# Optimization experiments

Hardware: AMD Instinct MI355X
Metric: run time of the kernel (lower is better)

## Reference

```python
import jax, jax.numpy as jnp
import numpy as np
from jax import lax

OUT = 24
THRESHOLD = 0.7
IOU_THRESHOLD = 0.5


def _conv(x, w, b):
    # x: [N,C,H,W], w: [O,I,kh,kw] (torch OIHW), valid padding, stride 1
    y = lax.conv_general_dilated(x, w, (1, 1), 'VALID',
                                 dimension_numbers=('NCHW', 'OIHW', 'NCHW'))
    return y + b[None, :, None, None]


def _prelu(x, a):
    a = a.reshape((1, -1) + (1,) * (x.ndim - 2))
    return jnp.where(x > 0, x, a * x)


def _maxpool(x, k, s, p):
    return lax.reduce_window(x, -jnp.inf, lax.max,
                             (1, 1, k, k), (1, 1, s, s),
                             [(0, 0), (0, 0), (p, p), (p, p)])


def _crop_resize(img, bboxes):
    # img: [3,H,W]; nearest-neighbor resize of each (clipped) crop to 24x24,
    # matching F.interpolate default nearest mode: src = floor(dst*in/out).
    _, H, W = img.shape
    x1 = jnp.clip(bboxes[:, 0].astype(jnp.int32), 0, W)
    y1 = jnp.clip(bboxes[:, 1].astype(jnp.int32), 0, H)
    x2 = jnp.clip(bboxes[:, 2].astype(jnp.int32), 0, W)
    y2 = jnp.clip(bboxes[:, 3].astype(jnp.int32), 0, H)
    j = jnp.arange(OUT)
    ix = jnp.clip(x1[:, None] + (j[None, :] * (x2 - x1)[:, None]) // OUT, 0, W - 1)  # [N,24]
    iy = jnp.clip(y1[:, None] + (j[None, :] * (y2 - y1)[:, None]) // OUT, 0, H - 1)  # [N,24]
    crops = img[:, iy[:, :, None], ix[:, None, :]]  # [3,N,24,24]
    return jnp.transpose(crops, (1, 0, 2, 3))        # [N,3,24,24]


def _pairwise_iou(b):
    x1 = jnp.maximum(b[:, None, 0], b[None, :, 0])
    y1 = jnp.maximum(b[:, None, 1], b[None, :, 1])
    x2 = jnp.minimum(b[:, None, 2], b[None, :, 2])
    y2 = jnp.minimum(b[:, None, 3], b[None, :, 3])
    inter = jnp.clip(x2 - x1, 0) * jnp.clip(y2 - y1, 0)
    area = jnp.clip(b[:, 2] - b[:, 0], 0) * jnp.clip(b[:, 3] - b[:, 1], 0)
    return inter / jnp.maximum(area[:, None] + area[None, :] - inter, 1e-12)


def _nms_keep(boxes, scores, valid, iou_thr):
    # Fixed-shape greedy NMS: returns boolean keep mask over original order.
    N = boxes.shape[0]
    order = jnp.argsort(-scores)
    b = boxes[order]
    v = valid[order]
    iou = _pairwise_iou(b)
    idx = jnp.arange(N)

    def body(i, supp):
        alive = v[i] & jnp.logical_not(supp[i])
        kill = alive & (iou[i] > iou_thr) & (idx > i)
        return supp | kill

    supp = lax.fori_loop(0, N, body, jnp.zeros((N,), bool))
    keep_sorted = v & jnp.logical_not(supp)
    return jnp.zeros((N,), bool).at[order].set(keep_sorted)


def _forward(image, bboxes, conv1_w, conv1_b, prelu1_a, conv2_w, conv2_b, prelu2_a,
             conv3_w, conv3_b, prelu3_a, lin4_w, lin4_b, prelu4_a,
             lin5a_w, lin5a_b, lin5b_w, lin5b_b):
    img = jnp.transpose((image - 127.5) * 0.0078125, (2, 0, 1))  # preprocess, HWC->CHW
    x = _crop_resize(img, bboxes)                                 # [N,3,24,24]
    x = _maxpool(_prelu(_conv(x, conv1_w, conv1_b), prelu1_a), 3, 2, 1)   # [N,28,11,11]
    x = _maxpool(_prelu(_conv(x, conv2_w, conv2_b), prelu2_a), 3, 2, 0)   # [N,48,4,4]
    x = _prelu(_conv(x, conv3_w, conv3_b), prelu3_a)                      # [N,64,3,3]
    x = x.reshape(x.shape[0], -1)                                          # [N,576]
    x = _prelu(x @ lin4_w.T + lin4_b, prelu4_a)                            # [N,128]
    cls = jax.nn.softmax(x @ lin5a_w.T + lin5a_b, axis=1)
    reg = x @ lin5b_w.T + lin5b_b
    scores = cls[:, 1]
    w = bboxes[:, 2] - bboxes[:, 0]
    h = bboxes[:, 3] - bboxes[:, 1]
    boxes = jnp.stack([bboxes[:, 0] + reg[:, 0] * w,
                       bboxes[:, 1] + reg[:, 1] * h,
                       bboxes[:, 2] + reg[:, 2] * w,
                       bboxes[:, 3] + reg[:, 3] * h], axis=1)
    return boxes, scores


def setup_inputs() -> dict:
    key = jax.random.key(0)
    ks = jax.random.split(key, 20)
    H, W, N = 1080, 1920, 4096
    image = jax.random.uniform(ks[0], (H, W, 3), jnp.float32, 0.0, 255.0)
    x1 = jax.random.randint(ks[1], (N,), 0, W - 96).astype(jnp.float32)
    y1 = jax.random.randint(ks[2], (N,), 0, H - 96).astype(jnp.float32)
    bw = jax.random.randint(ks[3], (N,), 24, 96).astype(jnp.float32)
    bh = jax.random.randint(ks[4], (N,), 24, 96).astype(jnp.float32)
    bboxes = jnp.stack([x1, y1, x1 + bw, y1 + bh], axis=1)

    def w(k, shape, scale):
        return jax.random.normal(k, shape, jnp.float32) * scale

    return dict(
        image=image, bboxes=bboxes,
        conv1_w=w(ks[5], (28, 3, 3, 3), 0.1), conv1_b=w(ks[6], (28,), 0.01),
        prelu1_a=jnp.full((28,), 0.25, jnp.float32),
        conv2_w=w(ks[7], (48, 28, 3, 3), 0.06), conv2_b=w(ks[8], (48,), 0.01),
        prelu2_a=jnp.full((48,), 0.25, jnp.float32),
        conv3_w=w(ks[9], (64, 48, 2, 2), 0.07), conv3_b=w(ks[10], (64,), 0.01),
        prelu3_a=jnp.full((64,), 0.25, jnp.float32),
        lin4_w=w(ks[11], (128, 576), 0.04), lin4_b=w(ks[12], (128,), 0.01),
        prelu4_a=jnp.full((128,), 0.25, jnp.float32),
        lin5a_w=w(ks[13], (2, 128), 0.2), lin5a_b=w(ks[14], (2,), 0.01),
        lin5b_w=w(ks[15], (4, 128), 0.09), lin5b_b=w(ks[16], (4,), 0.01),
    )


def reference(image, bboxes, conv1_w, conv1_b, prelu1_a, conv2_w, conv2_b, prelu2_a,
              conv3_w, conv3_b, prelu3_a, lin4_w, lin4_b, prelu4_a,
              lin5a_w, lin5a_b, lin5b_w, lin5b_b):
    boxes, scores = _forward(image, bboxes, conv1_w, conv1_b, prelu1_a,
                             conv2_w, conv2_b, prelu2_a, conv3_w, conv3_b, prelu3_a,
                             lin4_w, lin4_b, prelu4_a, lin5a_w, lin5a_b, lin5b_w, lin5b_b)
    valid = scores >= THRESHOLD
    keep = _nms_keep(boxes, scores, valid, IOU_THRESHOLD)
    # padded (masked) form of `bboxes[pick, :]` so output shape is static
    return jnp.where(keep[:, None], boxes, 0.0)
```

## Files before the change

### kernel.cpp

```cpp
#include <hip/hip_runtime.h>

typedef unsigned long long ull;
typedef __attribute__((ext_vector_type(8))) short bf16x8;
typedef __attribute__((ext_vector_type(4))) float f32x4;

#define W_IMG 1920
#define H_IMG 1080
#define NBOX 4096

#define S_CROP  0
#define S_WT1   2016
#define S_POOL1 5736
#define S_BUF2  3696
#define S_POOL2 7584
#define S_FEAT  0
#define S_VEC   576
#define S_LOUT  704
#define SMEM_F  9432

#define WS_BT   2277392

__device__ __forceinline__ float4 ld4(const float* p) { return *(const float4*)p; }
__device__ __forceinline__ float prelu_f(float v, float a) { return v > 0.f ? v : a * v; }
__device__ __forceinline__ unsigned short bf16rn(float v) {
  unsigned u = __float_as_uint(v);
  return (unsigned short)((u + 0x7fffu + ((u >> 16) & 1u)) >> 16);
}
__device__ __forceinline__ float bf16tof(unsigned short h) {
  return __uint_as_float(((unsigned)h) << 16);
}

__global__ __launch_bounds__(256) void wconv_kernel(const float* __restrict__ w2,
                                                    unsigned short* __restrict__ bt) {
  int tid = threadIdx.x;
  for (int e = tid; e < 13824; e += 256) {
    int c = e & 31, rest = e >> 5;
    int co = rest % 48, kk = rest / 48;
    float v = (c < 28) ? w2[co*252 + c*9 + kk] : 0.f;
    unsigned short h1 = bf16rn(v);
    unsigned short h2 = bf16rn(v - bf16tof(h1));
    bt[e] = h1;
    bt[13824 + e] = h2;
  }
}

template<int SHIFT, int PMIN>
__device__ __forceinline__ void conv1_pool_task(const float* sm, int cq, int y0, int a0,
                                                float* mx) {
#pragma unroll
  for (int wy = 0; wy < 3; ++wy) {
    int y = y0 + wy;
    if (y < 0) continue;
    float acc0[3] = {0.f,0.f,0.f}, acc1[3] = {0.f,0.f,0.f};
    float acc2[3] = {0.f,0.f,0.f}, acc3[3] = {0.f,0.f,0.f};
#pragma unroll
    for (int c = 0; c < 3; ++c) {
#pragma unroll
      for (int kyy = 0; kyy < 3; ++kyy) {
        float r[8];
        const float* src = sm + S_CROP + c*672 + (y + kyy)*28 + a0;
        *(float4*)&r[0] = ld4(src);
        *(float4*)&r[4] = ld4(src + 4);
#pragma unroll
        for (int kxx = 0; kxx < 3; ++kxx) {
          float4 wq = ld4(sm + S_WT1 + (c*9 + kyy*3 + kxx)*32 + cq*4);
#pragma unroll
          for (int wx = PMIN; wx < 3; ++wx) {
            float v = r[SHIFT + wx + kxx];
            acc0[wx] += v*wq.x; acc1[wx] += v*wq.y;
            acc2[wx] += v*wq.z; acc3[wx] += v*wq.w;
          }
        }
      }
    }
#pragma unroll
    for (int wx = PMIN; wx < 3; ++wx) {
      mx[0] = fmaxf(mx[0], acc0[wx]);
      mx[1] = fmaxf(mx[1], acc1[wx]);
      mx[2] = fmaxf(mx[2], acc2[wx]);
      mx[3] = fmaxf(mx[3], acc3[wx]);
    }
  }
}

__global__ __launch_bounds__(256, 4) void cnn_kernel(
    const float* __restrict__ image, const float* __restrict__ bboxes,
    const float* __restrict__ w1, const float* __restrict__ b1, const float* __restrict__ a1,
    const unsigned short* __restrict__ wbt,
    const float* __restrict__ b2, const float* __restrict__ a2,
    const float* __restrict__ w3, const float* __restrict__ b3, const float* __restrict__ a3,
    const float* __restrict__ w4, const float* __restrict__ b4, const float* __restrict__ a4,
    const float* __restrict__ w5a, const float* __restrict__ b5a,
    const float* __restrict__ w5b, const float* __restrict__ b5b,
    float* __restrict__ boxes, float* __restrict__ scores)
{
  __shared__ float sm[SMEM_F];
  __shared__ int s_ix[24], s_iy[24];
  const int tid = threadIdx.x;
  const int n = blockIdx.x;
  const float lo = -__builtin_inff();

  if (tid < 24) {
    int x1 = min(max((int)bboxes[n*4+0], 0), W_IMG);
    int x2 = min(max((int)bboxes[n*4+2], 0), W_IMG);
    s_ix[tid] = min(max(x1 + (tid*(x2-x1))/24, 0), W_IMG-1);
  } else if (tid >= 64 && tid < 88) {
    int j = tid - 64;
    int y1 = min(max((int)bboxes[n*4+1], 0), H_IMG);
    int y2 = min(max((int)bboxes[n*4+3], 0), H_IMG);
    s_iy[j] = min(max(y1 + (j*(y2-y1))/24, 0), H_IMG-1);
  }
  for (int d = tid; d < 756; d += 256) {
    int k = d / 28, co = d % 28;
    sm[S_WT1 + k*32 + co] = w1[co*27 + k];
  }
  __syncthreads();
  for (int e = tid; e < 1728; e += 256) {
    int c = e / 576, rr = e % 576, y = rr / 24, x = rr % 24;
    float v = image[(s_iy[y]*W_IMG + s_ix[x])*3 + c];
    sm[S_CROP + c*672 + y*28 + x] = (v - 127.5f) * 0.0078125f;
  }
  __syncthreads();

  {
    const int wv = tid >> 6, lane = tid & 63;
#pragma unroll 1
    for (int k = 0; k < 4; ++k) {
      const int s = 4*k + wv;
      float mx[4] = {lo, lo, lo, lo};
      int cq, py, px;
      bool valid;
      if (s < 7) {
        int idx = s*64 + lane;
        valid = idx < 385;
        cq = idx % 7; int q = idx / 7; if (q > 54) q = 54;
        py = q / 5; px = 2*(q % 5) + 1;
        conv1_pool_task<1,0>(sm, cq, 2*py - 1, (2*px - 1) & ~3, mx);
      } else if (s < 14) {
        int idx = (s - 7)*64 + lane;
        valid = idx < 385;
        cq = idx % 7; int q = idx / 7; if (q > 54) q = 54;
        py = q / 5; px = 2*(q % 5) + 2;
        conv1_pool_task<3,0>(sm, cq, 2*py - 1, (2*px - 1) & ~3, mx);
      } else {
        int idx = (s - 14)*64 + lane;
        valid = idx < 77;
        cq = idx % 7; py = idx / 7; if (py > 10) py = 10;
        px = 0;
        conv1_pool_task<-1,1>(sm, cq, 2*py - 1, 0, mx);
      }
      if (valid) {
        float4 bq = ld4(&b1[cq*4]);
        float4 aq = ld4(&a1[cq*4]);
        sm[S_POOL1 + (cq*4+0)*132 + py*12 + px] = prelu_f(mx[0] + bq.x, aq.x);
        sm[S_POOL1 + (cq*4+1)*132 + py*12 + px] = prelu_f(mx[1] + bq.y, aq.y);
        sm[S_POOL1 + (cq*4+2)*132 + py*12 + px] = prelu_f(mx[2] + bq.z, aq.z);
        sm[S_POOL1 + (cq*4+3)*132 + py*12 + px] = prelu_f(mx[3] + bq.w, aq.w);
      }
    }
  }
  __syncthreads();

  {
    unsigned short* pl = (unsigned short*)sm;
    for (int e = tid; e < 3696; e += 256) {
      float v = sm[S_POOL1 + e];
      int c = e / 132, rem = e - c*132;
      int it = rem*28 + c;
      unsigned short h1 = bf16rn(v);
      pl[it] = h1;
      pl[3696 + it] = bf16rn(v - bf16tof(h1));
    }
  }
  __syncthreads();

  {
    const int wv = tid >> 6, lane = tid & 63;
    const int grp = lane >> 4, lr = lane & 15;
    const unsigned short* pl = (const unsigned short*)sm;
    const bf16x8* bt = (const bf16x8*)wbt;
#pragma unroll 1
    for (int t = wv; t < 18; t += 4) {
      const int mtile = t / 3, ntile = t - 3*(t/3);
      const int co = ntile*16 + lr;
      const int arow = min(mtile*16 + lr, 80);
      const int oy = (arow*57) >> 9;
      const int ox = arow - 9*oy;
      const int pixb = (oy*12 + ox)*28 + grp*8;
      f32x4 acc = {0.f, 0.f, 0.f, 0.f};
#pragma unroll
      for (int kk = 0; kk < 9; ++kk) {
        const int ky = kk / 3, kx = kk - 3*(kk/3);
        const int aoff = pixb + (ky*12 + kx)*28;
        union { bf16x8 v; ull d[2]; } A1, A2;
        A1.d[0] = *(const ull*)(pl + aoff);
        A1.d[1] = *(const ull*)(pl + aoff + 4);
        A2.d[0] = *(const ull*)(pl + 3696 + aoff);
        A2.d[1] = *(const ull*)(pl + 3696 + aoff + 4);
        const bf16x8 B1 = bt[(kk*48 + co)*4 + grp];
        const bf16x8 B2 = bt[1728 + (kk*48 + co)*4 + grp];
        acc = __builtin_amdgcn_mfma_f32_16x16x32_bf16(A1.v, B2, acc, 0, 0, 0);
        acc = __builtin_amdgcn_mfma_f32_16x16x32_bf16(A2.v, B1, acc, 0, 0, 0);
        acc = __builtin_amdgcn_mfma_f32_16x16x32_bf16(A1.v, B1, acc, 0, 0, 0);
      }
      const float bb = b2[co], aa = a2[co];
      const int p0 = mtile*16 + grp*4;
#pragma unroll
      for (int r = 0; r < 4; ++r) {
        int p = p0 + r;
        if (p < 81) sm[S_BUF2 + co*81 + p] = prelu_f(acc[r] + bb, aa);
      }
    }
  }
  __syncthreads();

  for (int o = tid; o < 768; o += 256) {
    int cl = o >> 4, rem = o & 15, pyy = rem >> 2, pxx = rem & 3;
    float m = lo;
#pragma unroll
    for (int ky = 0; ky < 3; ++ky)
#pragma unroll
      for (int kx = 0; kx < 3; ++kx)
        m = fmaxf(m, sm[S_BUF2 + cl*81 + (2*pyy+ky)*9 + (2*pxx+kx)]);
    sm[S_POOL2 + o] = m;
  }
  __syncthreads();

  {
    int co = tid >> 2, c4 = tid & 3;
    float acc[9] = {};
    for (int cc = 0; cc < 12; ++cc) {
      int c = c4*12 + cc;
      float r[16];
      *(float4*)&r[0]  = ld4(sm + S_POOL2 + c*16);
      *(float4*)&r[4]  = ld4(sm + S_POOL2 + c*16 + 4);
      *(float4*)&r[8]  = ld4(sm + S_POOL2 + c*16 + 8);
      *(float4*)&r[12] = ld4(sm + S_POOL2 + c*16 + 12);
      float4 wq = ld4(&w3[co*192 + c*4]);
#pragma unroll
      for (int p = 0; p < 9; ++p) {
        int pyy = p / 3, pxx = p % 3;
        acc[p] += r[pyy*4+pxx]*wq.x + r[pyy*4+pxx+1]*wq.y
                + r[(pyy+1)*4+pxx]*wq.z + r[(pyy+1)*4+pxx+1]*wq.w;
      }
    }
#pragma unroll
    for (int p = 0; p < 9; ++p) {
      acc[p] += __shfl_xor(acc[p], 1, 64);
      acc[p] += __shfl_xor(acc[p], 2, 64);
    }
    if (c4 == 0) {
      float bb = b3[co], aa = a3[co];
#pragma unroll
      for (int p = 0; p < 9; ++p) sm[S_FEAT + co*9 + p] = prelu_f(acc[p] + bb, aa);
    }
  }
  __syncthreads();

  {
    int wv = tid >> 6, lane = tid & 63;
    for (int f = wv; f < 128; f += 4) {
      const float* wr = w4 + f*576;
      float acc = 0.f;
#pragma unroll
      for (int i = 0; i < 9; ++i) {
        int j = i*64 + lane;
        acc += wr[j] * sm[S_FEAT + j];
      }
#pragma unroll
      for (int off = 1; off < 64; off <<= 1) acc += __shfl_xor(acc, off, 64);
      if (lane == 0) sm[S_VEC + f] = prelu_f(acc + b4[f], a4[f]);
    }
  }
  __syncthreads();

  if (tid < 6) {
    const float* wr = (tid < 2) ? (w5a + tid*128) : (w5b + (tid-2)*128);
    float acc = 0.f;
#pragma unroll
    for (int j = 0; j < 32; ++j) {
      float4 xv = ld4(sm + S_VEC + j*4);
      float4 wv = ld4(wr + j*4);
      acc += xv.x*wv.x + xv.y*wv.y + xv.z*wv.z + xv.w*wv.w;
    }
    acc += (tid < 2) ? b5a[tid] : b5b[tid-2];
    sm[S_LOUT + tid] = acc;
  }
  __syncthreads();
  if (tid == 0) {
    float l0 = sm[S_LOUT+0], l1 = sm[S_LOUT+1];
    float m = fmaxf(l0, l1);
    float e0 = expf(l0 - m), e1 = expf(l1 - m);
    float sc = e1 / (e0 + e1);
    float4 bb = ld4(&bboxes[n*4]);
    float bw = bb.z - bb.x, bh = bb.w - bb.y;
    float4 ob = make_float4(bb.x + sm[S_LOUT+2]*bw, bb.y + sm[S_LOUT+3]*bh,
                            bb.z + sm[S_LOUT+4]*bw, bb.w + sm[S_LOUT+5]*bh);
    *(float4*)&boxes[n*4] = ob;
    scores[n] = sc;
  }
}

__global__ __launch_bounds__(1024) void sort_kernel(const float* __restrict__ scores,
                                                    const float* __restrict__ boxes,
                                                    int* __restrict__ order,
                                                    float* __restrict__ sboxes,
                                                    int* __restrict__ Vp) {
  __shared__ ull keys[NBOX];
  __shared__ int cnt;
  int tid = threadIdx.x;
  if (tid == 0) cnt = 0;
  __syncthreads();
  int local = 0;
  for (int i = tid; i < NBOX; i += 1024) {
    float s = scores[i];
    bool valid = (s >= 0.7f);
    unsigned hi = valid ? (0xFFFFFFFFu - __float_as_uint(s)) : 0xFFFFFFFFu;
    keys[i] = ((ull)hi << 32) | (unsigned)i;
    if (valid) local++;
  }
  atomicAdd(&cnt, local);
  __syncthreads();
  if (tid == 0) *Vp = cnt;
  if (cnt == 0) return;
  for (int k = 2; k <= NBOX; k <<= 1) {
    for (int j = k >> 1; j > 0; j >>= 1) {
      __syncthreads();
      for (int i = tid; i < NBOX; i += 1024) {
        int ij = i ^ j;
        if (ij > i) {
          ull a = keys[i], b = keys[ij];
          bool up = ((i & k) == 0);
          if ((a > b) == up) { keys[i] = b; keys[ij] = a; }
        }
      }
    }
  }
  __syncthreads();
  for (int i = tid; i < NBOX; i += 1024) {
    int idx = (int)(unsigned)(keys[i] & 0xFFFFFFFFu);
    order[i] = idx;
    *(float4*)&sboxes[i*4] = *(const float4*)&boxes[idx*4];
  }
}

__global__ __launch_bounds__(256) void iou_kernel(const float* __restrict__ sboxes,
                                                  const int* __restrict__ Vp,
                                                  ull* __restrict__ mask) {
  int i = blockIdx.x;
  int V = *Vp;
  if (i >= V) return;
  float4 bi = *(const float4*)&sboxes[i*4];
  float ai = fmaxf(bi.z - bi.x, 0.f) * fmaxf(bi.w - bi.y, 0.f);
  int lane = threadIdx.x & 63;
  for (int w = threadIdx.x >> 6; w < 64; w += 4) {
    int j = (w << 6) | lane;
    bool pred = false;
    if (j > i && j < V) {
      float4 bj = *(const float4*)&sboxes[j*4];
      float aj = fmaxf(bj.z - bj.x, 0.f) * fmaxf(bj.w - bj.y, 0.f);
      float xx1 = fmaxf(bi.x, bj.x), yy1 = fmaxf(bi.y, bj.y);
      float xx2 = fminf(bi.z, bj.z), yy2 = fminf(bi.w, bj.w);
      float inter = fmaxf(xx2 - xx1, 0.f) * fmaxf(yy2 - yy1, 0.f);
      float den = fmaxf(ai + aj - inter, 1e-12f);
      pred = (inter / den) > 0.5f;
    }
    ull bits = __ballot(pred);
    if (lane == 0) mask[(size_t)i*64 + w] = bits;
  }
}

#define CHUNK 16
__global__ __launch_bounds__(64) void nms_scan(const ull* __restrict__ mask,
                                               const int* __restrict__ Vp,
                                               const int* __restrict__ order,
                                               int* __restrict__ keep) {
  int lane = threadIdx.x;
  for (int idx = lane; idx < NBOX; idx += 64) keep[idx] = 0;
  __syncthreads();
  int V = *Vp;
  ull remw = 0;
  __shared__ ull buf[CHUNK][64];
  for (int base = 0; base < V; base += CHUNK) {
    int nn = min(CHUNK, V - base);
#pragma unroll
    for (int r = 0; r < CHUNK; ++r)
      if (r < nn) buf[r][lane] = mask[(size_t)(base + r)*64 + lane];
    for (int r = 0; r < nn; ++r) {
      int i = base + r;
      ull w = __shfl(remw, i >> 6, 64);
      if (!((w >> (i & 63)) & 1ull)) {
        remw |= buf[r][lane];
        if (lane == 0) keep[order[i]] = 1;
      }
    }
  }
}

__global__ __launch_bounds__(256) void out_kernel(const float* __restrict__ boxes,
                                                  const int* __restrict__ keep,
                                                  float* __restrict__ out) {
  int n = blockIdx.x * 256 + threadIdx.x;
  float4 b = *(const float4*)&boxes[n*4];
  float4 z = make_float4(0.f, 0.f, 0.f, 0.f);
  *(float4*)&out[n*4] = keep[n] ? b : z;
}

extern "C" void kernel_launch(void* const* d_in, const int* in_sizes, int n_in,
                              void* d_out, int out_size, void* d_ws, size_t ws_size,
                              hipStream_t stream) {
  const float* image  = (const float*)d_in[0];
  const float* bboxes = (const float*)d_in[1];
  const float* w1  = (const float*)d_in[2];
  const float* b1  = (const float*)d_in[3];
  const float* a1  = (const float*)d_in[4];
  const float* w2  = (const float*)d_in[5];
  const float* b2  = (const float*)d_in[6];
  const float* a2  = (const float*)d_in[7];
  const float* w3  = (const float*)d_in[8];
  const float* b3  = (const float*)d_in[9];
  const float* a3  = (const float*)d_in[10];
  const float* w4  = (const float*)d_in[11];
  const float* b4  = (const float*)d_in[12];
  const float* a4  = (const float*)d_in[13];
  const float* w5a = (const float*)d_in[14];
  const float* b5a = (const float*)d_in[15];
  const float* w5b = (const float*)d_in[16];
  const float* b5b = (const float*)d_in[17];

  char* ws = (char*)d_ws;
  float* boxes  = (float*)(ws + 0);
  float* scores = (float*)(ws + 65536);
  float* sboxes = (float*)(ws + 81920);
  int*   order  = (int*)  (ws + 147456);
  int*   Vp     = (int*)  (ws + 163840);
  int*   keep   = (int*)  (ws + 163856);
  ull*   mask   = (ull*)  (ws + 180240);
  unsigned short* wbt = (unsigned short*)(ws + WS_BT);

  float* out = (float*)d_out;

  wconv_kernel<<<1, 256, 0, stream>>>(w2, wbt);
  cnn_kernel<<<NBOX, 256, 0, stream>>>(image, bboxes, w1,b1,a1, wbt, b2,a2, w3,b3,a3,
                                       w4,b4,a4, w5a,b5a, w5b,b5b, boxes, scores);
  sort_kernel<<<1, 1024, 0, stream>>>(scores, boxes, order, sboxes, Vp);
  iou_kernel<<<NBOX, 256, 0, stream>>>(sboxes, Vp, mask);
  nms_scan<<<1, 64, 0, stream>>>(mask, Vp, order, keep);
  out_kernel<<<16, 256, 0, stream>>>(boxes, keep, out);
}
```

Baseline: 410.2 us.

## Move conv1 onto bf16 MFMA with split-precision and chunked pooling

```diff
diff --git a/kernel.cpp b/kernel.cpp
--- a/kernel.cpp
+++ b/kernel.cpp
@@ -8,17 +8,18 @@
 #define H_IMG 1080
 #define NBOX 4096
 
-#define S_CROP  0
-#define S_WT1   2016
-#define S_POOL1 5736
-#define S_BUF2  3696
-#define S_POOL2 7584
-#define S_FEAT  0
-#define S_VEC   576
-#define S_LOUT  704
-#define SMEM_F  9432
-
-#define WS_BT   2277392
+#define S_CROP   0
+#define S_CBUF   2016
+#define S_PLANES 5152
+#define S_BUF2   0
+#define S_POOL2  3888
+#define S_FEAT   0
+#define S_VEC    576
+#define S_LOUT   704
+#define SMEM_F   8848
+
+#define WS_BT    2277392
+#define WS_BT1   2332688
 
 __device__ __forceinline__ float4 ld4(const float* p) { return *(const float4*)p; }
 __device__ __forceinline__ float prelu_f(float v, float a) { return v > 0.f ? v : a * v; }
@@ -31,61 +32,36 @@
 }
 
 __global__ __launch_bounds__(256) void wconv_kernel(const float* __restrict__ w2,
-                                                    unsigned short* __restrict__ bt) {
-  int tid = threadIdx.x;
-  for (int e = tid; e < 13824; e += 256) {
-    int c = e & 31, rest = e >> 5;
-    int co = rest % 48, kk = rest / 48;
-    float v = (c < 28) ? w2[co*252 + c*9 + kk] : 0.f;
-    unsigned short h1 = bf16rn(v);
-    unsigned short h2 = bf16rn(v - bf16tof(h1));
-    bt[e] = h1;
-    bt[13824 + e] = h2;
-  }
-}
-
-template<int SHIFT, int PMIN>
-__device__ __forceinline__ void conv1_pool_task(const float* sm, int cq, int y0, int a0,
-                                                float* mx) {
-#pragma unroll
-  for (int wy = 0; wy < 3; ++wy) {
-    int y = y0 + wy;
-    if (y < 0) continue;
-    float acc0[3] = {0.f,0.f,0.f}, acc1[3] = {0.f,0.f,0.f};
-    float acc2[3] = {0.f,0.f,0.f}, acc3[3] = {0.f,0.f,0.f};
-#pragma unroll
-    for (int c = 0; c < 3; ++c) {
-#pragma unroll
-      for (int kyy = 0; kyy < 3; ++kyy) {
-        float r[8];
-        const float* src = sm + S_CROP + c*672 + (y + kyy)*28 + a0;
-        *(float4*)&r[0] = ld4(src);
-        *(float4*)&r[4] = ld4(src + 4);
-#pragma unroll
-        for (int kxx = 0; kxx < 3; ++kxx) {
-          float4 wq = ld4(sm + S_WT1 + (c*9 + kyy*3 + kxx)*32 + cq*4);
-#pragma unroll
-          for (int wx = PMIN; wx < 3; ++wx) {
-            float v = r[SHIFT + wx + kxx];
-            acc0[wx] += v*wq.x; acc1[wx] += v*wq.y;
-            acc2[wx] += v*wq.z; acc3[wx] += v*wq.w;
-          }
-        }
-      }
-    }
-#pragma unroll
-    for (int wx = PMIN; wx < 3; ++wx) {
-      mx[0] = fmaxf(mx[0], acc0[wx]);
-      mx[1] = fmaxf(mx[1], acc1[wx]);
-      mx[2] = fmaxf(mx[2], acc2[wx]);
-      mx[3] = fmaxf(mx[3], acc3[wx]);
+                                                    const float* __restrict__ w1,
+                                                    unsigned short* __restrict__ bt,
+                                                    unsigned short* __restrict__ bt1) {
+  int b = blockIdx.x, tid = threadIdx.x;
+  if (b < 16) {
+    for (int e = b*864 + tid; e < (b+1)*864; e += 256) {
+      int c = e & 31, rest = e >> 5;
+      int co = rest % 48, kk = rest / 48;
+      float v = (c < 28) ? w2[co*252 + c*9 + kk] : 0.f;
+      unsigned short h1 = bf16rn(v);
+      bt[e] = h1;
+      bt[13824 + e] = bf16rn(v - bf16tof(h1));
+    }
+  } else {
+    for (int e = tid; e < 2048; e += 256) {
+      int j = e & 7, rest = e >> 3;
+      int co = rest & 31, pg = rest >> 5;
+      int grp = pg & 3, plane = pg >> 2;
+      int k = grp*8 + j;
+      float v = (k < 27 && co < 28) ? w1[co*27 + k] : 0.f;
+      unsigned short h1 = bf16rn(v);
+      bt1[e] = plane ? bf16rn(v - bf16tof(h1)) : h1;
     }
   }
 }
 
 __global__ __launch_bounds__(256, 4) void cnn_kernel(
     const float* __restrict__ image, const float* __restrict__ bboxes,
-    const float* __restrict__ w1, const float* __restrict__ b1, const float* __restrict__ a1,
+    const unsigned short* __restrict__ wbt1,
+    const float* __restrict__ b1, const float* __restrict__ a1,
     const unsigned short* __restrict__ wbt,
     const float* __restrict__ b2, const float* __restrict__ a2,
     const float* __restrict__ w3, const float* __restrict__ b3, const float* __restrict__ a3,
@@ -99,6 +75,24 @@
   const int tid = threadIdx.x;
   const int n = blockIdx.x;
   const float lo = -__builtin_inff();
+  const int lane = tid & 63, wv = tid >> 6;
+  const int grp = lane >> 4, lr = lane & 15;
+
+  bf16x8 c1B[2][2];
+  {
+    const bf16x8* btc = (const bf16x8*)wbt1;
+    c1B[0][0] = btc[(0*4 + grp)*32 + lr];
+    c1B[0][1] = btc[(0*4 + grp)*32 + 16 + lr];
+    c1B[1][0] = btc[(1*4 + grp)*32 + lr];
+    c1B[1][1] = btc[(1*4 + grp)*32 + 16 + lr];
+  }
+  int aoff[8];
+#pragma unroll
+  for (int j = 0; j < 8; ++j) {
+    int k = grp*8 + j;
+    int c = k / 9, rr = k - 9*c, ky = rr / 3, kx = rr - 3*ky;
+    aoff[j] = c*672 + ky*28 + kx;
+  }
 
   if (tid < 24) {
     int x1 = min(max((int)bboxes[n*4+0], 0), W_IMG);
@@ -110,10 +104,6 @@
     int y2 = min(max((int)bboxes[n*4+3], 0), H_IMG);
     s_iy[j] = min(max(y1 + (j*(y2-y1))/24, 0), H_IMG-1);
   }
-  for (int d = tid; d < 756; d += 256) {
-    int k = d / 28, co = d % 28;
-    sm[S_WT1 + k*32 + co] = w1[co*27 + k];
-  }
   __syncthreads();
   for (int e = tid; e < 1728; e += 256) {
     int c = e / 576, rr = e % 576, y = rr / 24, x = rr % 24;
@@ -123,61 +113,80 @@
   __syncthreads();
 
   {
-    const int wv = tid >> 6, lane = tid & 63;
+    unsigned short* cb = (unsigned short*)(sm + S_CBUF);
+    unsigned short* pl = (unsigned short*)(sm + S_PLANES);
+    const int c_r0[3] = {0, 7, 15};
+    const int c_R [3] = {8, 9, 7};
+    const int c_p0[3] = {0, 4, 8};
+    const int c_np[3] = {4, 4, 3};
 #pragma unroll 1
-    for (int k = 0; k < 4; ++k) {
-      const int s = 4*k + wv;
-      float mx[4] = {lo, lo, lo, lo};
-      int cq, py, px;
-      bool valid;
-      if (s < 7) {
-        int idx = s*64 + lane;
-        valid = idx < 385;
-        cq = idx % 7; int q = idx / 7; if (q > 54) q = 54;
-        py = q / 5; px = 2*(q % 5) + 1;
-        conv1_pool_task<1,0>(sm, cq, 2*py - 1, (2*px - 1) & ~3, mx);
-      } else if (s < 14) {
-        int idx = (s - 7)*64 + lane;
-        valid = idx < 385;
-        cq = idx % 7; int q = idx / 7; if (q > 54) q = 54;
-        py = q / 5; px = 2*(q % 5) + 2;
-        conv1_pool_task<3,0>(sm, cq, 2*py - 1, (2*px - 1) & ~3, mx);
-      } else {
-        int idx = (s - 14)*64 + lane;
-        valid = idx < 77;
-        cq = idx % 7; py = idx / 7; if (py > 10) py = 10;
-        px = 0;
-        conv1_pool_task<-1,1>(sm, cq, 2*py - 1, 0, mx);
-      }
-      if (valid) {
-        float4 bq = ld4(&b1[cq*4]);
-        float4 aq = ld4(&a1[cq*4]);
-        sm[S_POOL1 + (cq*4+0)*132 + py*12 + px] = prelu_f(mx[0] + bq.x, aq.x);
-        sm[S_POOL1 + (cq*4+1)*132 + py*12 + px] = prelu_f(mx[1] + bq.y, aq.y);
-        sm[S_POOL1 + (cq*4+2)*132 + py*12 + px] = prelu_f(mx[2] + bq.z, aq.z);
-        sm[S_POOL1 + (cq*4+3)*132 + py*12 + px] = prelu_f(mx[3] + bq.w, aq.w);
-      }
-    }
-  }
-  __syncthreads();
+    for (int ck = 0; ck < 3; ++ck) {
+      const int r0 = c_r0[ck], R = c_R[ck], p0 = c_p0[ck], np = c_np[ck];
+      const int npix = R*22;
+      const int mt = (npix + 15) >> 4;
+#pragma unroll 1
+      for (int t = wv; t < mt; t += 4) {
+        int row = t*16 + lr;
+        int pix = min(row, npix - 1);
+        int ly = pix / 22;
+        int x  = pix - ly*22;
+        int base = (r0 + ly)*28 + x;
+        unsigned short h1[8], h2[8];
+#pragma unroll
+        for (int j = 0; j < 8; ++j) {
+          float v = 0.f;
+          if (grp*8 + j < 27) v = sm[base + aoff[j]];
+          h1[j] = bf16rn(v);
+          h2[j] = bf16rn(v - bf16tof(h1[j]));
+        }
+        union { bf16x8 v; unsigned u[4]; } A1, A2;
+#pragma unroll
+        for (int q = 0; q < 4; ++q) {
+          A1.u[q] = (unsigned)h1[2*q] | ((unsigned)h1[2*q+1] << 16);
+          A2.u[q] = (unsigned)h2[2*q] | ((unsigned)h2[2*q+1] << 16);
+        }
+        f32x4 acc0 = {0.f,0.f,0.f,0.f}, acc1 = {0.f,0.f,0.f,0.f};
+        acc0 = __builtin_amdgcn_mfma_f32_16x16x32_bf16(A1.v, c1B[1][0], acc0, 0, 0, 0);
+        acc0 = __builtin_amdgcn_mfma_f32_16x16x32_bf16(A2.v, c1B[0][0], acc0, 0, 0, 0);
+        acc0 = __builtin_amdgcn_mfma_f32_16x16x32_bf16(A1.v, c1B[0][0], acc0, 0, 0, 0);
+        acc1 = __builtin_amdgcn_mfma_f32_16x16x32_bf16(A1.v, c1B[1][1], acc1, 0, 0, 0);
+        acc1 = __builtin_amdgcn_mfma_f32_16x16x32_bf16(A2.v, c1B[0][1], acc1, 0, 0, 0);
+        acc1 = __builtin_amdgcn_mfma_f32_16x16x32_bf16(A1.v, c1B[0][1], acc1, 0, 0, 0);
+        int p0r = t*16 + grp*4;
+        union { ull d; unsigned short s[4]; } W;
+#pragma unroll
+        for (int r = 0; r < 4; ++r) W.s[r] = bf16rn(acc0[r]);
+        *(ull*)(cb + lr*224 + p0r) = W.d;
+        if (lr < 12) {
+#pragma unroll
+          for (int r = 0; r < 4; ++r) W.s[r] = bf16rn(acc1[r]);
+          *(ull*)(cb + (16 + lr)*224 + p0r) = W.d;
+        }
+      }
+      __syncthreads();
+      const int npt = np * 308;
+      for (int o = tid; o < npt; o += 256) {
+        int pyl = o / 308, rem = o - pyl*308;
+        int co = rem / 11, px = rem - co*11;
+        int py = p0 + pyl;
+        int rlo = max(2*py - 1, 0) - r0, rhi = 2*py + 1 - r0;
+        int clo = max(2*px - 1, 0), chi = min(2*px + 1, 21);
+        float m = lo;
+        for (int r = rlo; r <= rhi; ++r)
+          for (int c2 = clo; c2 <= chi; ++c2)
+            m = fmaxf(m, bf16tof(cb[co*224 + r*22 + c2]));
+        float v = prelu_f(m + b1[co], a1[co]);
+        unsigned short g1 = bf16rn(v);
+        int it = (py*12 + px)*28 + co;
+        pl[it] = g1;
+        pl[3696 + it] = bf16rn(v - bf16tof(g1));
+      }
+      __syncthreads();
+    }
+  }
 
   {
-    unsigned short* pl = (unsigned short*)sm;
-    for (int e = tid; e < 3696; e += 256) {
-      float v = sm[S_POOL1 + e];
-      int c = e / 132, rem = e - c*132;
-      int it = rem*28 + c;
-      unsigned short h1 = bf16rn(v);
-      pl[it] = h1;
-      pl[3696 + it] = bf16rn(v - bf16tof(h1));
-    }
-  }
-  __syncthreads();
-
-  {
-    const int wv = tid >> 6, lane = tid & 63;
-    const int grp = lane >> 4, lr = lane & 15;
-    const unsigned short* pl = (const unsigned short*)sm;
+    const unsigned short* pl = (const unsigned short*)(sm + S_PLANES);
     const bf16x8* bt = (const bf16x8*)wbt;
 #pragma unroll 1
     for (int t = wv; t < 18; t += 4) {
@@ -191,12 +200,12 @@
 #pragma unroll
       for (int kk = 0; kk < 9; ++kk) {
         const int ky = kk / 3, kx = kk - 3*(kk/3);
-        const int aoff = pixb + (ky*12 + kx)*28;
+        const int aoff2 = pixb + (ky*12 + kx)*28;
         union { bf16x8 v; ull d[2]; } A1, A2;
-        A1.d[0] = *(const ull*)(pl + aoff);
-        A1.d[1] = *(const ull*)(pl + aoff + 4);
-        A2.d[0] = *(const ull*)(pl + 3696 + aoff);
-        A2.d[1] = *(const ull*)(pl + 3696 + aoff + 4);
+        A1.d[0] = *(const ull*)(pl + aoff2);
+        A1.d[1] = *(const ull*)(pl + aoff2 + 4);
+        A2.d[0] = *(const ull*)(pl + 3696 + aoff2);
+        A2.d[1] = *(const ull*)(pl + 3696 + aoff2 + 4);
         const bf16x8 B1 = bt[(kk*48 + co)*4 + grp];
         const bf16x8 B2 = bt[1728 + (kk*48 + co)*4 + grp];
         acc = __builtin_amdgcn_mfma_f32_16x16x32_bf16(A1.v, B2, acc, 0, 0, 0);
@@ -258,7 +267,6 @@
   __syncthreads();
 
   {
-    int wv = tid >> 6, lane = tid & 63;
     for (int f = wv; f < 128; f += 4) {
       const float* wr = w4 + f*576;
       float acc = 0.f;
@@ -436,12 +444,13 @@
   int*   Vp     = (int*)  (ws + 163840);
   int*   keep   = (int*)  (ws + 163856);
   ull*   mask   = (ull*)  (ws + 180240);
-  unsigned short* wbt = (unsigned short*)(ws + WS_BT);
+  unsigned short* wbt  = (unsigned short*)(ws + WS_BT);
+  unsigned short* wbt1 = (unsigned short*)(ws + WS_BT1);
 
   float* out = (float*)d_out;
 
-  wconv_kernel<<<1, 256, 0, stream>>>(w2, wbt);
-  cnn_kernel<<<NBOX, 256, 0, stream>>>(image, bboxes, w1,b1,a1, wbt, b2,a2, w3,b3,a3,
+  wconv_kernel<<<17, 256, 0, stream>>>(w2, w1, wbt, wbt1);
+  cnn_kernel<<<NBOX, 256, 0, stream>>>(image, bboxes, wbt1, b1,a1, wbt, b2,a2, w3,b3,a3,
                                        w4,b4,a4, w5a,b5a, w5b,b5b, boxes, scores);
   sort_kernel<<<1, 1024, 0, stream>>>(scores, boxes, order, sboxes, Vp);
   iou_kernel<<<NBOX, 256, 0, stream>>>(sboxes, Vp, mask);
```

Measured after the change: 399.0 us. 2.7% less time.
